# Performance work log

Hardware: AMD Instinct MI355X
Metric: run time of the kernel (lower is better)

The kernel has to match this reference:

```python
import jax, jax.numpy as jnp
import numpy as np

D_MODEL, N_HEADS, D_STATE, N_GROUPS, CHUNK = 2048, 32, 64, 1, 256
BATCH, SEQLEN = 2, 4096


def setup_inputs() -> dict:
    key = jax.random.key(0)
    ks = jax.random.split(key, 8)
    s = 0.02
    d, h, n, g = D_MODEL, N_HEADS, D_STATE, N_GROUPS
    return {
        "x": jax.random.normal(ks[0], (BATCH, SEQLEN, d), jnp.float32),
        "A_log": jnp.log(jnp.arange(1, h + 1, dtype=jnp.float32)),
        "D": jnp.ones((h,), jnp.float32),
        "B_w": jax.random.normal(ks[1], (g * n, d), jnp.float32) * s,
        "B_b": jnp.zeros((g * n,), jnp.float32),
        "C_w": jax.random.normal(ks[2], (g * n, d), jnp.float32) * s,
        "C_b": jnp.zeros((g * n,), jnp.float32),
        "dt_w": jax.random.normal(ks[3], (h, d), jnp.float32) * s,
        "dt_b": jnp.zeros((h,), jnp.float32),
        "out_w": jax.random.normal(ks[4], (d, d), jnp.float32) * s,
        "out_b": jnp.zeros((d,), jnp.float32),
    }


def segsum(v):
    # v: [..., T] -> [..., T, T]; out[i,j] = sum_{k=j+1..i} v[k] for i>=j, -inf else
    cs = jnp.cumsum(v, axis=-1)
    seg = cs[..., :, None] - cs[..., None, :]
    T = v.shape[-1]
    mask = jnp.tril(jnp.ones((T, T), bool))
    return jnp.where(mask, seg, -jnp.inf)


def _ssd(x, A_log, D, B_w, B_b, C_w, C_b, dt_w, dt_b, out_w, out_b):
    b, t, d = x.shape
    h = A_log.shape[0]
    n = B_w.shape[0] // N_GROUPS
    p = d // h
    l = CHUNK
    c = t // l

    A = -jnp.exp(A_log.astype(jnp.float32))                      # [h]
    B = (x @ B_w.T + B_b).reshape(b, t, N_GROUPS, n)             # g=1
    C = (x @ C_w.T + C_b).reshape(b, t, N_GROUPS, n)
    B = jnp.broadcast_to(B, (b, t, h, n))                        # repeat groups -> heads
    C = jnp.broadcast_to(C, (b, t, h, n))
    dt = jax.nn.softplus(x @ dt_w.T + dt_b)                      # [b,t,h]
    xh = x.reshape(b, t, h, p)

    # chunked SSD (Mamba2 mamba_chunk_scan_combined math)
    xc = xh.reshape(b, c, l, h, p)
    Bc = B.reshape(b, c, l, h, n)
    Cc = C.reshape(b, c, l, h, n)
    dtc = dt.reshape(b, c, l, h)
    dA = jnp.transpose(dtc * A, (0, 3, 1, 2))                    # [b,h,c,l]
    A_cumsum = jnp.cumsum(dA, axis=-1)                           # [b,h,c,l]

    # 1. intra-chunk (diagonal blocks)
    L = jnp.exp(segsum(dA))                                      # [b,h,c,l,l]
    xdt = xc * dtc[..., None]                                    # [b,c,l,h,p]
    Y_diag = jnp.einsum('bclhn,bcshn,bhcls,bcshp->bclhp', Cc, Bc, L, xdt)

    # 2. per-chunk final states
    decay_states = jnp.exp(A_cumsum[..., -1:] - A_cumsum)        # [b,h,c,l]
    states = jnp.einsum('bclhn,bhcl,bclhp->bchpn', Bc, decay_states, xdt)

    # 3. inter-chunk recurrence on chunk states
    states = jnp.concatenate([jnp.zeros_like(states[:, :1]), states], axis=1)  # [b,c+1,h,p,n]
    dA_last = jnp.pad(A_cumsum[..., -1], ((0, 0), (0, 0), (1, 0)))             # [b,h,c+1]
    decay_chunk = jnp.exp(segsum(dA_last))                                     # [b,h,c+1,c+1]
    new_states = jnp.einsum('bhzc,bchpn->bzhpn', decay_chunk, states)
    prev_states = new_states[:, :-1]                                           # [b,c,h,p,n]

    # 4. state -> output contribution
    state_decay_out = jnp.exp(A_cumsum)                          # [b,h,c,l]
    Y_off = jnp.einsum('bclhn,bchpn,bhcl->bclhp', Cc, prev_states, state_decay_out)

    Y = (Y_diag + Y_off).reshape(b, t, h, p) + D[None, None, :, None] * xh
    return Y.reshape(b, t, d) @ out_w.T + out_b


def reference(x, A_log, D, B_w, B_b, C_w, C_b, dt_w, dt_b, out_w, out_b):
    return _ssd(x, A_log, D, B_w, B_b, C_w, C_b, dt_w, dt_b, out_w, out_b)
```

## Files before the change

kernel.cpp:

```cpp
#include <hip/hip_runtime.h>
#include <hip/hip_bf16.h>
#include <math.h>

namespace {
constexpr int kDModel = 2048;
constexpr int kHeads  = 32;
constexpr int kState  = 64;
constexpr int kP      = 64;
constexpr int kChunk  = 256;
constexpr int kNChunk = 16;
constexpr int kBatch  = 2;
constexpr int kSeq    = 4096;
constexpr int kM      = kBatch * kSeq;
}

typedef __bf16 bf16_t;
typedef __attribute__((ext_vector_type(8))) __bf16 bf16x8;
typedef __attribute__((ext_vector_type(4))) __bf16 bf16x4;
typedef __attribute__((ext_vector_type(4))) float f32x4;

__device__ __forceinline__ void gload_lds16(const void* g, void* l) {
    __builtin_amdgcn_global_load_lds(
        (const __attribute__((address_space(1))) void*)g,
        (__attribute__((address_space(3))) void*)l,
        16, 0, 0);
}

__global__ __launch_bounds__(256)
void gemm_bcdt(const float* __restrict__ x, const bf16_t* __restrict__ W,
               const float* __restrict__ b0, const float* __restrict__ b1,
               const float* __restrict__ b2,
               bf16_t* __restrict__ o0h, bf16_t* __restrict__ o1h,
               float* __restrict__ o2f)
{
    constexpr int K = kDModel;
    constexpr int NT = K / 32;
    __shared__ float  Ast[3][256 * 4];
    __shared__ __bf16 Wst[3][768 * 8];
    const int tid  = threadIdx.x;
    const int lane = tid & 63;
    const int wave = tid >> 6;
    const int wm = (wave >> 1) * 16;
    const int wn = (wave & 1) * 80;
    const int l15 = lane & 15, quad = lane >> 4;
    const int m0 = blockIdx.x * 32;
    const int aks = tid >> 5, arow = tid & 31;

    auto stage = [&](int t2, int sb) {
        const int k0 = t2 * 32;
        gload_lds16(x + (size_t)(m0 + arow) * K + k0 + aks * 4, &Ast[sb][tid * 4]);
        #pragma unroll
        for (int e = 0; e < 3; ++e) {
            const int u = e * 256 + tid;
            const int ks = u / 192;
            const int n  = u - ks * 192;
            gload_lds16(W + (size_t)n * K + k0 + ks * 8, &Wst[sb][u * 8]);
        }
    };

    f32x4 acc[5];
    #pragma unroll
    for (int j = 0; j < 5; ++j) acc[j] = (f32x4){0.f, 0.f, 0.f, 0.f};

    stage(0, 0);
    stage(1, 1);
    asm volatile("s_waitcnt vmcnt(4)" ::: "memory");
    __builtin_amdgcn_s_barrier();

    int cur = 0;
    for (int t = 0; t < NT; ++t) {
        const float*  Ac = &Ast[cur][0];
        const __bf16* Wc = &Wst[cur][0];
        int stb = cur + 2; if (stb >= 3) stb -= 3;

        const float4 a0 = *reinterpret_cast<const float4*>(
            &Ac[((quad * 2 + 0) * 32 + wm + l15) * 4]);
        const float4 a1 = *reinterpret_cast<const float4*>(
            &Ac[((quad * 2 + 1) * 32 + wm + l15) * 4]);
        bf16x8 af;
        af[0] = (__bf16)a0.x; af[1] = (__bf16)a0.y;
        af[2] = (__bf16)a0.z; af[3] = (__bf16)a0.w;
        af[4] = (__bf16)a1.x; af[5] = (__bf16)a1.y;
        af[6] = (__bf16)a1.z; af[7] = (__bf16)a1.w;
        bf16x8 bfr[5];
        #pragma unroll
        for (int nf = 0; nf < 5; ++nf)
            bfr[nf] = *reinterpret_cast<const bf16x8*>(
                &Wc[(quad * 192 + wn + nf * 16 + l15) * 8]);
        if (t < NT - 2) stage(t + 2, stb);
        __builtin_amdgcn_s_setprio(1);
        #pragma unroll
        for (int nf = 0; nf < 5; ++nf)
            acc[nf] = __builtin_amdgcn_mfma_f32_16x16x32_bf16(af, bfr[nf], acc[nf], 0, 0, 0);
        __builtin_amdgcn_s_setprio(0);

        if (t < NT - 2) {
            asm volatile("s_waitcnt vmcnt(4)" ::: "memory");
        } else if (t < NT - 1) {
            asm volatile("s_waitcnt vmcnt(0)" ::: "memory");
        }
        if (t < NT - 1) __builtin_amdgcn_s_barrier();
        cur = cur + 1; if (cur == 3) cur = 0;
    }

    #pragma unroll
    for (int reg = 0; reg < 4; ++reg) {
        const int r = m0 + wm + quad * 4 + reg;
        #pragma unroll
        for (int nf = 0; nf < 5; ++nf) {
            const float v = acc[nf][reg];
            const int n = wn + nf * 16 + l15;
            if (n < 64) {
                o0h[(size_t)r * 64 + n] = (bf16_t)(v + b0[n]);
            } else if (n < 128) {
                o1h[(size_t)r * 64 + (n - 64)] = (bf16_t)(v + b1[n - 64]);
            } else {
                float z = v + b2[n - 128];
                o2f[(size_t)r * 32 + (n - 128)] = (z > 20.f) ? z : log1pf(expf(z));
            }
        }
    }
}

__global__ __launch_bounds__(512, 2)
void gemm256_out(const bf16_t* __restrict__ Ap, const bf16_t* __restrict__ Bp,
                 const float* __restrict__ bias, float* __restrict__ C)
{
    constexpr int M = 8192, N = 2048, NT = 2048 / 32;
    __shared__ __bf16 Ab[3][4 * 256 * 8];
    __shared__ __bf16 Bb[3][4 * 256 * 8];
    const int tid  = threadIdx.x;
    const int lane = tid & 63;
    const int wave = tid >> 6;
    const int l15 = lane & 15, quad = lane >> 4;
    const int bid = blockIdx.x;
    const int mt = (bid & 7) * 4 + ((bid >> 3) & 3);
    const int nt = bid >> 5;
    const int m0 = mt * 256;
    const int n0 = nt * 256;
    const int wm = (wave >> 2) * 128;
    const int wn = (wave & 3) * 64;

    const int u0 = tid, u1 = tid + 512;
    auto stage = [&](int t2, int stb) {
        const int ks0 = t2 * 4;
        const bf16_t* As = Ap + ((size_t)ks0 * M + m0) * 8;
        const bf16_t* Bs = Bp + ((size_t)ks0 * N + n0) * 8;
        __bf16* Al = &Ab[stb][0];
        __bf16* Bl = &Bb[stb][0];
        gload_lds16(As + ((size_t)(u0 >> 8) * M + (u0 & 255)) * 8, Al + u0 * 8);
        gload_lds16(As + ((size_t)(u1 >> 8) * M + (u1 & 255)) * 8, Al + u1 * 8);
        gload_lds16(Bs + ((size_t)(u0 >> 8) * N + (u0 & 255)) * 8, Bl + u0 * 8);
        gload_lds16(Bs + ((size_t)(u1 >> 8) * N + (u1 & 255)) * 8, Bl + u1 * 8);
    };

    f32x4 acc[8][4];
    #pragma unroll
    for (int i = 0; i < 8; ++i)
        #pragma unroll
        for (int j = 0; j < 4; ++j)
            acc[i][j] = (f32x4){0.f, 0.f, 0.f, 0.f};

    stage(0, 0);
    stage(1, 1);
    asm volatile("s_waitcnt vmcnt(4)" ::: "memory");
    __builtin_amdgcn_s_barrier();

    int cur = 0;
    for (int t = 0; t < NT; ++t) {
        const __bf16* Ac = &Ab[cur][0];
        const __bf16* Bc = &Bb[cur][0];
        int stb = cur + 2; if (stb >= 3) stb -= 3;

        bf16x8 af[4], bfr[4];
        #pragma unroll
        for (int mi = 0; mi < 4; ++mi)
            af[mi] = *reinterpret_cast<const bf16x8*>(
                &Ac[(quad * 256 + wm + mi * 16 + l15) * 8]);
        #pragma unroll
        for (int nj = 0; nj < 4; ++nj)
            bfr[nj] = *reinterpret_cast<const bf16x8*>(
                &Bc[(quad * 256 + wn + nj * 16 + l15) * 8]);
        if (t < NT - 2) stage(t + 2, stb);
        __builtin_amdgcn_s_setprio(1);
        #pragma unroll
        for (int mi = 0; mi < 4; ++mi)
            #pragma unroll
            for (int nj = 0; nj < 4; ++nj)
                acc[mi][nj] = __builtin_amdgcn_mfma_f32_16x16x32_bf16(
                    af[mi], bfr[nj], acc[mi][nj], 0, 0, 0);
        __builtin_amdgcn_s_setprio(0);

        #pragma unroll
        for (int mi = 0; mi < 4; ++mi)
            af[mi] = *reinterpret_cast<const bf16x8*>(
                &Ac[(quad * 256 + wm + 64 + mi * 16 + l15) * 8]);
        __builtin_amdgcn_s_setprio(1);
        #pragma unroll
        for (int mi = 0; mi < 4; ++mi)
            #pragma unroll
            for (int nj = 0; nj < 4; ++nj)
                acc[4 + mi][nj] = __builtin_amdgcn_mfma_f32_16x16x32_bf16(
                    af[mi], bfr[nj], acc[4 + mi][nj], 0, 0, 0);
        __builtin_amdgcn_s_setprio(0);

        if (t < NT - 2) {
            asm volatile("s_waitcnt vmcnt(4)" ::: "memory");
        } else if (t < NT - 1) {
            asm volatile("s_waitcnt vmcnt(0)" ::: "memory");
        }
        if (t < NT - 1) __builtin_amdgcn_s_barrier();
        cur = cur + 1; if (cur == 3) cur = 0;
    }

    float bia[4];
    #pragma unroll
    for (int nj = 0; nj < 4; ++nj) bia[nj] = bias[n0 + wn + nj * 16 + l15];
    #pragma unroll
    for (int mi = 0; mi < 8; ++mi) {
        #pragma unroll
        for (int reg = 0; reg < 4; ++reg) {
            const int r = m0 + wm + mi * 16 + quad * 4 + reg;
            #pragma unroll
            for (int nj = 0; nj < 4; ++nj) {
                const int c = n0 + wn + nj * 16 + l15;
                C[(size_t)r * N + c] = acc[mi][nj][reg] + bia[nj];
            }
        }
    }
}

__global__ __launch_bounds__(256)
void prep_fused(const float* __restrict__ W, bf16_t* __restrict__ Wp,
                const float* __restrict__ B_w, const float* __restrict__ C_w,
                const float* __restrict__ dt_w, bf16_t* __restrict__ wcat)
{
    const int bid = blockIdx.x;
    if (bid < 2048) {
        const int idx = bid * 256 + threadIdx.x;
        const int n = idx >> 8, ks = idx & 255;
        const float4 v0 = *reinterpret_cast<const float4*>(W + (size_t)n * 2048 + ks * 8);
        const float4 v1 = *reinterpret_cast<const float4*>(W + (size_t)n * 2048 + ks * 8 + 4);
        bf16x8 o;
        o[0] = (__bf16)v0.x; o[1] = (__bf16)v0.y; o[2] = (__bf16)v0.z; o[3] = (__bf16)v0.w;
        o[4] = (__bf16)v1.x; o[5] = (__bf16)v1.y; o[6] = (__bf16)v1.z; o[7] = (__bf16)v1.w;
        *reinterpret_cast<bf16x8*>(Wp + ((size_t)ks * 2048 + n) * 8) = o;
    } else {
        const int idx = (bid - 2048) * 256 + threadIdx.x;
        const int r = idx >> 11, k = idx & 2047;
        float v = 0.f;
        if (r < 64)       v = B_w[r * 2048 + k];
        else if (r < 128) v = C_w[(r - 64) * 2048 + k];
        else if (r < 160) v = dt_w[(r - 128) * 2048 + k];
        wcat[idx] = (bf16_t)v;
    }
}

__global__ __launch_bounds__(256)
void mid_fused(const float* __restrict__ dtm, const float* __restrict__ A_log,
               float* __restrict__ Acs, const bf16_t* __restrict__ Bb16,
               bf16_t* __restrict__ bTg, const float* __restrict__ x,
               bf16_t* __restrict__ xdtT)
{
    const int bid = blockIdx.x;
    const int tid = threadIdx.x;
    if (bid < 1024) {
        const int ci = bid & (kNChunk - 1);
        const int hi = (bid >> 4) & (kHeads - 1);
        const int bi = bid >> 9;
        const float Ah = -expf(A_log[hi]);
        __shared__ float s[kChunk];
        s[tid] = dtm[((size_t)bi * kSeq + ci * kChunk + tid) * kHeads + hi] * Ah;
        __syncthreads();
        for (int off = 1; off < kChunk; off <<= 1) {
            const float add = (tid >= off) ? s[tid - off] : 0.f;
            __syncthreads();
            s[tid] += add;
            __syncthreads();
        }
        Acs[((size_t)(bi * kHeads + hi) * kNChunk + ci) * kChunk + tid] = s[tid];
    } else if (bid < 1024 + 32) {
        const int blk = bid - 1024;
        const int ci = blk & (kNChunk - 1);
        const int bi = blk >> 4;
        const size_t rowbase = (size_t)bi * kSeq + ci * kChunk;
        __shared__ __bf16 T[64 * 264];
        bf16x8 v[8];
        #pragma unroll
        for (int e = 0; e < 8; ++e)
            v[e] = *reinterpret_cast<const bf16x8*>(Bb16 + (rowbase + tid) * 64 + e * 8);
        #pragma unroll
        for (int e = 0; e < 8; ++e)
            #pragma unroll
            for (int j = 0; j < 8; ++j)
                T[(e * 8 + j) * 264 + tid] = v[e][j];
        __syncthreads();
        const int n = tid >> 2, seg = (tid & 3) * 64;
        bf16_t* dst = bTg + ((size_t)(bi * kNChunk + ci)) * (64 * 256) + n * 256 + seg;
        #pragma unroll
        for (int j = 0; j < 8; ++j) {
            *reinterpret_cast<bf16x8*>(dst + j * 8) =
                *reinterpret_cast<const bf16x8*>(&T[n * 264 + seg + j * 8]);
        }
    } else {
        const int blk = bid - 1024 - 32;
        const int hi = blk & (kHeads - 1);
        const int ci = (blk >> 5) & (kNChunk - 1);
        const int bi = blk >> 9;
        const size_t rowbase = (size_t)bi * kSeq + ci * kChunk;
        __shared__ __bf16 T[64 * 264];
        const float d = dtm[(rowbase + tid) * kHeads + hi];
        const float* xs = x + (rowbase + tid) * kDModel + hi * kP;
        #pragma unroll
        for (int e = 0; e < 8; ++e) {
            const float4 a = *reinterpret_cast<const float4*>(xs + e * 8);
            const float4 b = *reinterpret_cast<const float4*>(xs + e * 8 + 4);
            T[(e * 8 + 0) * 264 + tid] = (__bf16)(a.x * d);
            T[(e * 8 + 1) * 264 + tid] = (__bf16)(a.y * d);
            T[(e * 8 + 2) * 264 + tid] = (__bf16)(a.z * d);
            T[(e * 8 + 3) * 264 + tid] = (__bf16)(a.w * d);
            T[(e * 8 + 4) * 264 + tid] = (__bf16)(b.x * d);
            T[(e * 8 + 5) * 264 + tid] = (__bf16)(b.y * d);
            T[(e * 8 + 6) * 264 + tid] = (__bf16)(b.z * d);
            T[(e * 8 + 7) * 264 + tid] = (__bf16)(b.w * d);
        }
        __syncthreads();
        const int p = tid >> 2, seg = (tid & 3) * 64;
        bf16_t* dst = xdtT + (size_t)blk * (64 * 256) + p * 256 + seg;
        #pragma unroll
        for (int j = 0; j < 8; ++j) {
            *reinterpret_cast<bf16x8*>(dst + j * 8) =
                *reinterpret_cast<const bf16x8*>(&T[p * 264 + seg + j * 8]);
        }
    }
}

__global__ __launch_bounds__(256)
void states_mfma(const bf16_t* __restrict__ xdtT, const bf16_t* __restrict__ bTg,
                 const float* __restrict__ Acs, float* __restrict__ states)
{
    const int blk = blockIdx.x;
    const int hi = blk & (kHeads - 1);
    const int ci = (blk >> 5) & (kNChunk - 1);
    const int bi = blk >> 9;
    __shared__ __bf16 Xa[64 * 264];
    __shared__ __bf16 Bt[64 * 264];
    __shared__ float dec[kChunk];
    const int tid = threadIdx.x;
    const int lane = tid & 63;
    const int wave = tid >> 6;
    const int l15 = lane & 15, quad = lane >> 4;

    const float* acs = Acs + ((size_t)(bi * kHeads + hi) * kNChunk + ci) * kChunk;
    dec[tid] = expf(acs[kChunk - 1] - acs[tid]);
    __syncthreads();

    const bf16_t* bsrc = bTg + ((size_t)(bi * kNChunk + ci)) * (64 * 256);
    const bf16_t* xsrc = xdtT + (size_t)blk * (64 * 256);
    #pragma unroll
    for (int e = 0; e < 8; ++e) {
        const int u = e * 256 + tid;
        const int r = u >> 5, seg = (u & 31) * 8;
        *reinterpret_cast<bf16x8*>(&Bt[r * 264 + seg]) =
            *reinterpret_cast<const bf16x8*>(bsrc + r * 256 + seg);
        bf16x8 xv = *reinterpret_cast<const bf16x8*>(xsrc + r * 256 + seg);
        bf16x8 xo;
        #pragma unroll
        for (int j = 0; j < 8; ++j)
            xo[j] = (__bf16)((float)xv[j] * dec[seg + j]);
        *reinterpret_cast<bf16x8*>(&Xa[r * 264 + seg]) = xo;
    }
    __syncthreads();

    f32x4 acc[4];
    #pragma unroll
    for (int ni = 0; ni < 4; ++ni) acc[ni] = (f32x4){0.f, 0.f, 0.f, 0.f};
    #pragma unroll
    for (int kk = 0; kk < 8; ++kk) {
        const bf16x8 af = *reinterpret_cast<const bf16x8*>(
            &Xa[(wave * 16 + l15) * 264 + kk * 32 + quad * 8]);
        #pragma unroll
        for (int ni = 0; ni < 4; ++ni) {
            const bf16x8 bf = *reinterpret_cast<const bf16x8*>(
                &Bt[(ni * 16 + l15) * 264 + kk * 32 + quad * 8]);
            acc[ni] = __builtin_amdgcn_mfma_f32_16x16x32_bf16(af, bf, acc[ni], 0, 0, 0);
        }
    }
    float* sp = states + (size_t)blk * (kP * kState);
    #pragma unroll
    for (int reg = 0; reg < 4; ++reg) {
        const int p = wave * 16 + quad * 4 + reg;
        #pragma unroll
        for (int ni = 0; ni < 4; ++ni)
            sp[(size_t)p * kState + ni * 16 + l15] = acc[ni][reg];
    }
}

__global__ __launch_bounds__(256)
void chunkscan_kernel(const float* __restrict__ states, const float* __restrict__ Acs,
                      bf16_t* __restrict__ prevsb)
{
    const int q  = blockIdx.x & 15;
    const int hi = (blockIdx.x >> 4) & (kHeads - 1);
    const int bi = blockIdx.x >> 9;
    const int e  = q * 256 + threadIdx.x;
    __shared__ float ea[kNChunk];
    if (threadIdx.x < kNChunk)
        ea[threadIdx.x] = expf(Acs[((size_t)(bi * kHeads + hi) * kNChunk + threadIdx.x)
                                   * kChunk + kChunk - 1]);
    __syncthreads();
    float P = 0.f;
    prevsb[((size_t)(bi * kNChunk + 0) * kHeads + hi) * (kP * kState) + e] = (bf16_t)0.f;
    for (int c = 1; c < kNChunk; ++c) {
        P = fmaf(ea[c - 1], P,
                 states[((size_t)(bi * kNChunk + (c - 1)) * kHeads + hi) * (kP * kState) + e]);
        prevsb[((size_t)(bi * kNChunk + c) * kHeads + hi) * (kP * kState) + e] = (bf16_t)P;
    }
}

__global__ __launch_bounds__(256)
void ychunk_mfma(const bf16_t* __restrict__ Bb16, const bf16_t* __restrict__ Cb16,
                 const bf16_t* __restrict__ xdtT, const float* __restrict__ Acs,
                 const bf16_t* __restrict__ prevsb, const float* __restrict__ dtm,
                 const float* __restrict__ Dvec, bf16_t* __restrict__ Yp)
{
    const int blk = blockIdx.x;
    const int lt = blk & 3;
    const int hi = (blk >> 2) & (kHeads - 1);
    const int ci = (blk >> 7) & (kNChunk - 1);
    const int bi = blk >> 11;
    __shared__ float acs_s[kChunk];
    __shared__ float dts_s[64];
    __shared__ __bf16 Cs[64 * 72];
    __shared__ __bf16 Bs[64 * 72];
    __shared__ __bf16 Xt[64 * 72];
    __shared__ __bf16 Sp[64 * 72];
    const int tid = threadIdx.x;
    const int lane = tid & 63;
    const int wave = tid >> 6;
    const int l15 = lane & 15, quad = lane >> 4;
    const int mrow = wave * 16 + quad * 4;
    const size_t rowbase = (size_t)bi * kSeq + ci * kChunk;
    const bf16_t* xdsrc = xdtT + ((size_t)((bi * kNChunk + ci) * kHeads + hi)) * (64 * 256);
    const int ur0 = tid >> 3,          useg0 = (tid & 7) * 8;
    const int ur1 = (256 + tid) >> 3,  useg1 = (tid & 7) * 8;

    acs_s[tid] = Acs[((size_t)(bi * kHeads + hi) * kNChunk + ci) * kChunk + tid];
    if (tid < 64) dts_s[tid] = dtm[(rowbase + lt * 64 + tid) * kHeads + hi];
    const bf16_t* pp = prevsb + ((size_t)(bi * kNChunk + ci) * kHeads + hi) * (kP * kState);
    #pragma unroll
    for (int e = 0; e < 2; ++e) {
        const int r = e ? ur1 : ur0, seg = e ? useg1 : useg0;
        *reinterpret_cast<bf16x8*>(&Cs[r * 72 + seg]) =
            *reinterpret_cast<const bf16x8*>(Cb16 + (rowbase + lt * 64 + r) * 64 + seg);
        *reinterpret_cast<bf16x8*>(&Bs[r * 72 + seg]) =
            *reinterpret_cast<const bf16x8*>(pp + r * 64 + seg);
    }
    bf16x8 rB0, rB1, rX0, rX1;
    rB0 = *reinterpret_cast<const bf16x8*>(Bb16 + (rowbase + ur0) * 64 + useg0);
    rB1 = *reinterpret_cast<const bf16x8*>(Bb16 + (rowbase + ur1) * 64 + useg1);
    rX0 = *reinterpret_cast<const bf16x8*>(xdsrc + ur0 * 256 + useg0);
    rX1 = *reinterpret_cast<const bf16x8*>(xdsrc + ur1 * 256 + useg1);
    __syncthreads();

    bf16x8 af[2];
    af[0] = *reinterpret_cast<const bf16x8*>(&Cs[(wave * 16 + l15) * 72 + quad * 8]);
    af[1] = *reinterpret_cast<const bf16x8*>(&Cs[(wave * 16 + l15) * 72 + 32 + quad * 8]);

    f32x4 yacc[4];
    #pragma unroll
    for (int ni = 0; ni < 4; ++ni) yacc[ni] = (f32x4){0.f, 0.f, 0.f, 0.f};
    #pragma unroll
    for (int ni = 0; ni < 4; ++ni) {
        const bf16x8 b0 = *reinterpret_cast<const bf16x8*>(&Bs[(ni * 16 + l15) * 72 + quad * 8]);
        const bf16x8 b1 = *reinterpret_cast<const bf16x8*>(&Bs[(ni * 16 + l15) * 72 + 32 + quad * 8]);
        yacc[ni] = __builtin_amdgcn_mfma_f32_16x16x32_bf16(af[0], b0, yacc[ni], 0, 0, 0);
        yacc[ni] = __builtin_amdgcn_mfma_f32_16x16x32_bf16(af[1], b1, yacc[ni], 0, 0, 0);
    }
    {
        float es[4];
        #pragma unroll
        for (int reg = 0; reg < 4; ++reg) es[reg] = expf(acs_s[lt * 64 + mrow + reg]);
        #pragma unroll
        for (int ni = 0; ni < 4; ++ni)
            #pragma unroll
            for (int reg = 0; reg < 4; ++reg) yacc[ni][reg] *= es[reg];
    }

    for (int st = 0; st <= lt; ++st) {
        __syncthreads();
        *reinterpret_cast<bf16x8*>(&Bs[ur0 * 72 + useg0]) = rB0;
        *reinterpret_cast<bf16x8*>(&Bs[ur1 * 72 + useg1]) = rB1;
        *reinterpret_cast<bf16x8*>(&Xt[ur0 * 72 + useg0]) = rX0;
        *reinterpret_cast<bf16x8*>(&Xt[ur1 * 72 + useg1]) = rX1;
        if (st < lt) {
            rB0 = *reinterpret_cast<const bf16x8*>(Bb16 + (rowbase + (st + 1) * 64 + ur0) * 64 + useg0);
            rB1 = *reinterpret_cast<const bf16x8*>(Bb16 + (rowbase + (st + 1) * 64 + ur1) * 64 + useg1);
            rX0 = *reinterpret_cast<const bf16x8*>(xdsrc + ur0 * 256 + (st + 1) * 64 + useg0);
            rX1 = *reinterpret_cast<const bf16x8*>(xdsrc + ur1 * 256 + (st + 1) * 64 + useg1);
        }
        __syncthreads();
        f32x4 sacc[4];
        #pragma unroll
        for (int ni = 0; ni < 4; ++ni) sacc[ni] = (f32x4){0.f, 0.f, 0.f, 0.f};
        #pragma unroll
        for (int ni = 0; ni < 4; ++ni) {
            const bf16x8 b0 = *reinterpret_cast<const bf16x8*>(&Bs[(ni * 16 + l15) * 72 + quad * 8]);
            const bf16x8 b1 = *reinterpret_cast<const bf16x8*>(&Bs[(ni * 16 + l15) * 72 + 32 + quad * 8]);
            sacc[ni] = __builtin_amdgcn_mfma_f32_16x16x32_bf16(af[0], b0, sacc[ni], 0, 0, 0);
            sacc[ni] = __builtin_amdgcn_mfma_f32_16x16x32_bf16(af[1], b1, sacc[ni], 0, 0, 0);
        }
        #pragma unroll
        for (int reg = 0; reg < 4; ++reg) {
            const int l = lt * 64 + mrow + reg;
            const float al = acs_s[l];
            #pragma unroll
            for (int ni = 0; ni < 4; ++ni) {
                const int scol = ni * 16 + l15;
                const int sg = st * 64 + scol;
                float v = sacc[ni][reg] * expf(al - acs_s[sg]);
                if (st == lt && sg > l) v = 0.f;
                Sp[(mrow + reg) * 72 + scol] = (__bf16)v;
            }
        }
        asm volatile("s_waitcnt lgkmcnt(0)" ::: "memory");
        __builtin_amdgcn_sched_barrier(0);
        const bf16x8 as0 = *reinterpret_cast<const bf16x8*>(&Sp[(wave * 16 + l15) * 72 + quad * 8]);
        const bf16x8 as1 = *reinterpret_cast<const bf16x8*>(&Sp[(wave * 16 + l15) * 72 + 32 + quad * 8]);
        #pragma unroll
        for (int ni = 0; ni < 4; ++ni) {
            const bf16x8 x0 = *reinterpret_cast<const bf16x8*>(&Xt[(ni * 16 + l15) * 72 + quad * 8]);
            const bf16x8 x1 = *reinterpret_cast<const bf16x8*>(&Xt[(ni * 16 + l15) * 72 + 32 + quad * 8]);
            yacc[ni] = __builtin_amdgcn_mfma_f32_16x16x32_bf16(as0, x0, yacc[ni], 0, 0, 0);
            yacc[ni] = __builtin_amdgcn_mfma_f32_16x16x32_bf16(as1, x1, yacc[ni], 0, 0, 0);
        }
    }

    const float Dh = Dvec[hi];
    #pragma unroll
    for (int reg = 0; reg < 4; ++reg) {
        const int lrow = mrow + reg;
        const size_t tg = rowbase + lt * 64 + lrow;
        const float dinv = 1.f / dts_s[lrow];
        #pragma unroll
        for (int ni = 0; ni < 4; ++ni) {
            const int p = ni * 16 + l15;
            const float xv = (float)Xt[p * 72 + lrow] * dinv;
            const float v = yacc[ni][reg] + Dh * xv;
            Yp[((size_t)(hi * 8 + (p >> 3)) * (size_t)kM + tg) * 8 + (p & 7)] = (bf16_t)v;
        }
    }
}

extern "C" void kernel_launch(void* const* d_in, const int* in_sizes, int n_in,
                              void* d_out, int out_size, void* d_ws, size_t ws_size,
                              hipStream_t stream)
{
    (void)in_sizes; (void)n_in; (void)out_size; (void)ws_size;
    const float* x     = (const float*)d_in[0];
    const float* A_log = (const float*)d_in[1];
    const float* Dvec  = (const float*)d_in[2];
    const float* B_w   = (const float*)d_in[3];
    const float* B_b   = (const float*)d_in[4];
    const float* C_w   = (const float*)d_in[5];
    const float* C_b   = (const float*)d_in[6];
    const float* dt_w  = (const float*)d_in[7];
    const float* dt_b  = (const float*)d_in[8];
    const float* out_w = (const float*)d_in[9];
    const float* out_b = (const float*)d_in[10];
    float* out = (float*)d_out;

    float* ws = (float*)d_ws;
    float* dtm    = ws;
    float* Acs    = dtm + (size_t)kM * kHeads;
    float* states = Acs + (size_t)kBatch * kHeads * kNChunk * kChunk;
    bf16_t* prevsb = (bf16_t*)(states + (size_t)kBatch * kNChunk * kHeads * kP * kState);
    bf16_t* Y     = prevsb + (size_t)kBatch * kNChunk * kHeads * kP * kState;
    bf16_t* Bb16  = Y + (size_t)kM * kDModel;
    bf16_t* Cb16  = Bb16 + (size_t)kM * kState;
    bf16_t* xdtT  = Cb16 + (size_t)kM * kState;
    bf16_t* bTg   = xdtT + (size_t)kM * kDModel;
    bf16_t* wcat  = bTg + (size_t)kBatch * kNChunk * kState * kChunk;
    bf16_t* wob   = wcat + (size_t)192 * kDModel;

    const dim3 blk(256);
    prep_fused<<<dim3(2048 + 1536), blk, 0, stream>>>(out_w, wob, B_w, C_w, dt_w, wcat);
    gemm_bcdt<<<dim3(kM / 32), blk, 0, stream>>>(x, wcat, B_b, C_b, dt_b,
                                                 Bb16, Cb16, dtm);
    mid_fused<<<dim3(1024 + 32 + 1024), blk, 0, stream>>>(
        dtm, A_log, Acs, Bb16, bTg, x, xdtT);
    states_mfma<<<dim3(kBatch * kNChunk * kHeads), blk, 0, stream>>>(xdtT, bTg, Acs, states);
    chunkscan_kernel<<<dim3(kBatch * kHeads * 16), blk, 0, stream>>>(states, Acs, prevsb);
    ychunk_mfma<<<dim3(kBatch * kNChunk * kHeads * 4), blk, 0, stream>>>(
        Bb16, Cb16, xdtT, Acs, prevsb, dtm, Dvec, Y);
    gemm256_out<<<dim3(256), dim3(512), 0, stream>>>(Y, wob, out_b, out);
}
```

Before: 350.6 us.

## Merge four ychunk row-tile blocks into one 512-thread block sharing B/X tiles

ychunk_mfma now launches one 512-thread block per (batch, chunk, head) instead of four 256-thread blocks, one per 64-row tile. Each pair of waves owns one 64-row tile. The B and xdt tiles for each source sub-chunk are staged into LDS once and shared by all row tiles, which removes the redundant global loads the separate blocks used to make. The C tile buffer is reused as the scratch for the masked score matrix. In exchange, waves for early row tiles sit idle through later source steps but still hit every barrier, and the grid has four times fewer blocks.

```diff
diff --git a/kernel.cpp b/kernel.cpp
--- a/kernel.cpp
+++ b/kernel.cpp
@@ -418,136 +418,158 @@
     }
 }
 
-__global__ __launch_bounds__(256)
+__global__ __launch_bounds__(512)
 void ychunk_mfma(const bf16_t* __restrict__ Bb16, const bf16_t* __restrict__ Cb16,
                  const bf16_t* __restrict__ xdtT, const float* __restrict__ Acs,
                  const bf16_t* __restrict__ prevsb, const float* __restrict__ dtm,
                  const float* __restrict__ Dvec, bf16_t* __restrict__ Yp)
 {
     const int blk = blockIdx.x;
-    const int lt = blk & 3;
-    const int hi = (blk >> 2) & (kHeads - 1);
-    const int ci = (blk >> 7) & (kNChunk - 1);
-    const int bi = blk >> 11;
+    const int hi = blk & (kHeads - 1);
+    const int ci = (blk >> 5) & (kNChunk - 1);
+    const int bi = blk >> 9;
     __shared__ float acs_s[kChunk];
-    __shared__ float dts_s[64];
-    __shared__ __bf16 Cs[64 * 72];
-    __shared__ __bf16 Bs[64 * 72];
+    __shared__ float dts_s[kChunk];
+    __shared__ __bf16 CsSp[256 * 72];
+    __shared__ __bf16 BsPs[64 * 72];
     __shared__ __bf16 Xt[64 * 72];
-    __shared__ __bf16 Sp[64 * 72];
     const int tid = threadIdx.x;
     const int lane = tid & 63;
     const int wave = tid >> 6;
+    const int lt   = wave >> 1;
+    const int half = wave & 1;
     const int l15 = lane & 15, quad = lane >> 4;
-    const int mrow = wave * 16 + quad * 4;
+    const int rbase = lt * 64 + half * 32;
     const size_t rowbase = (size_t)bi * kSeq + ci * kChunk;
-    const bf16_t* xdsrc = xdtT + ((size_t)((bi * kNChunk + ci) * kHeads + hi)) * (64 * 256);
-    const int ur0 = tid >> 3,          useg0 = (tid & 7) * 8;
-    const int ur1 = (256 + tid) >> 3,  useg1 = (tid & 7) * 8;
-
-    acs_s[tid] = Acs[((size_t)(bi * kHeads + hi) * kNChunk + ci) * kChunk + tid];
-    if (tid < 64) dts_s[tid] = dtm[(rowbase + lt * 64 + tid) * kHeads + hi];
+    const bf16_t* xdsrc = xdtT + (size_t)blk * (64 * 256);
+    const int ur = tid >> 3, useg = (tid & 7) * 8;
+
+    if (tid < 256) acs_s[tid] = Acs[((size_t)(bi * kHeads + hi) * kNChunk + ci) * kChunk + tid];
+    else           dts_s[tid - 256] = dtm[(rowbase + tid - 256) * kHeads + hi];
+    #pragma unroll
+    for (int e = 0; e < 4; ++e) {
+        const int u = e * 512 + tid;
+        const int r = u >> 3, seg = (u & 7) * 8;
+        *reinterpret_cast<bf16x8*>(&CsSp[r * 72 + seg]) =
+            *reinterpret_cast<const bf16x8*>(Cb16 + (rowbase + r) * 64 + seg);
+    }
     const bf16_t* pp = prevsb + ((size_t)(bi * kNChunk + ci) * kHeads + hi) * (kP * kState);
-    #pragma unroll
-    for (int e = 0; e < 2; ++e) {
-        const int r = e ? ur1 : ur0, seg = e ? useg1 : useg0;
-        *reinterpret_cast<bf16x8*>(&Cs[r * 72 + seg]) =
-            *reinterpret_cast<const bf16x8*>(Cb16 + (rowbase + lt * 64 + r) * 64 + seg);
-        *reinterpret_cast<bf16x8*>(&Bs[r * 72 + seg]) =
-            *reinterpret_cast<const bf16x8*>(pp + r * 64 + seg);
-    }
-    bf16x8 rB0, rB1, rX0, rX1;
-    rB0 = *reinterpret_cast<const bf16x8*>(Bb16 + (rowbase + ur0) * 64 + useg0);
-    rB1 = *reinterpret_cast<const bf16x8*>(Bb16 + (rowbase + ur1) * 64 + useg1);
-    rX0 = *reinterpret_cast<const bf16x8*>(xdsrc + ur0 * 256 + useg0);
-    rX1 = *reinterpret_cast<const bf16x8*>(xdsrc + ur1 * 256 + useg1);
+    *reinterpret_cast<bf16x8*>(&BsPs[ur * 72 + useg]) =
+        *reinterpret_cast<const bf16x8*>(pp + ur * 64 + useg);
+    bf16x8 rB, rX;
+    rB = *reinterpret_cast<const bf16x8*>(Bb16 + (rowbase + ur) * 64 + useg);
+    rX = *reinterpret_cast<const bf16x8*>(xdsrc + ur * 256 + useg);
     __syncthreads();
 
-    bf16x8 af[2];
-    af[0] = *reinterpret_cast<const bf16x8*>(&Cs[(wave * 16 + l15) * 72 + quad * 8]);
-    af[1] = *reinterpret_cast<const bf16x8*>(&Cs[(wave * 16 + l15) * 72 + 32 + quad * 8]);
-
-    f32x4 yacc[4];
-    #pragma unroll
-    for (int ni = 0; ni < 4; ++ni) yacc[ni] = (f32x4){0.f, 0.f, 0.f, 0.f};
+    bf16x8 af[2][2];
+    #pragma unroll
+    for (int mi = 0; mi < 2; ++mi) {
+        af[mi][0] = *reinterpret_cast<const bf16x8*>(&CsSp[(rbase + mi * 16 + l15) * 72 + quad * 8]);
+        af[mi][1] = *reinterpret_cast<const bf16x8*>(&CsSp[(rbase + mi * 16 + l15) * 72 + 32 + quad * 8]);
+    }
+
+    f32x4 yacc[2][4];
+    #pragma unroll
+    for (int mi = 0; mi < 2; ++mi)
+        #pragma unroll
+        for (int ni = 0; ni < 4; ++ni) yacc[mi][ni] = (f32x4){0.f, 0.f, 0.f, 0.f};
     #pragma unroll
     for (int ni = 0; ni < 4; ++ni) {
-        const bf16x8 b0 = *reinterpret_cast<const bf16x8*>(&Bs[(ni * 16 + l15) * 72 + quad * 8]);
-        const bf16x8 b1 = *reinterpret_cast<const bf16x8*>(&Bs[(ni * 16 + l15) * 72 + 32 + quad * 8]);
-        yacc[ni] = __builtin_amdgcn_mfma_f32_16x16x32_bf16(af[0], b0, yacc[ni], 0, 0, 0);
-        yacc[ni] = __builtin_amdgcn_mfma_f32_16x16x32_bf16(af[1], b1, yacc[ni], 0, 0, 0);
-    }
-    {
+        const bf16x8 b0 = *reinterpret_cast<const bf16x8*>(&BsPs[(ni * 16 + l15) * 72 + quad * 8]);
+        const bf16x8 b1 = *reinterpret_cast<const bf16x8*>(&BsPs[(ni * 16 + l15) * 72 + 32 + quad * 8]);
+        #pragma unroll
+        for (int mi = 0; mi < 2; ++mi) {
+            yacc[mi][ni] = __builtin_amdgcn_mfma_f32_16x16x32_bf16(af[mi][0], b0, yacc[mi][ni], 0, 0, 0);
+            yacc[mi][ni] = __builtin_amdgcn_mfma_f32_16x16x32_bf16(af[mi][1], b1, yacc[mi][ni], 0, 0, 0);
+        }
+    }
+    #pragma unroll
+    for (int mi = 0; mi < 2; ++mi) {
         float es[4];
         #pragma unroll
-        for (int reg = 0; reg < 4; ++reg) es[reg] = expf(acs_s[lt * 64 + mrow + reg]);
+        for (int reg = 0; reg < 4; ++reg)
+            es[reg] = expf(acs_s[rbase + mi * 16 + quad * 4 + reg]);
         #pragma unroll
         for (int ni = 0; ni < 4; ++ni)
             #pragma unroll
-            for (int reg = 0; reg < 4; ++reg) yacc[ni][reg] *= es[reg];
-    }
-
-    for (int st = 0; st <= lt; ++st) {
+            for (int reg = 0; reg < 4; ++reg) yacc[mi][ni][reg] *= es[reg];
+    }
+
+    const float Dh = Dvec[hi];
+    for (int st = 0; st < 4; ++st) {
         __syncthreads();
-        *reinterpret_cast<bf16x8*>(&Bs[ur0 * 72 + useg0]) = rB0;
-        *reinterpret_cast<bf16x8*>(&Bs[ur1 * 72 + useg1]) = rB1;
-        *reinterpret_cast<bf16x8*>(&Xt[ur0 * 72 + useg0]) = rX0;
-        *reinterpret_cast<bf16x8*>(&Xt[ur1 * 72 + useg1]) = rX1;
-        if (st < lt) {
-            rB0 = *reinterpret_cast<const bf16x8*>(Bb16 + (rowbase + (st + 1) * 64 + ur0) * 64 + useg0);
-            rB1 = *reinterpret_cast<const bf16x8*>(Bb16 + (rowbase + (st + 1) * 64 + ur1) * 64 + useg1);
-            rX0 = *reinterpret_cast<const bf16x8*>(xdsrc + ur0 * 256 + (st + 1) * 64 + useg0);
-            rX1 = *reinterpret_cast<const bf16x8*>(xdsrc + ur1 * 256 + (st + 1) * 64 + useg1);
+        *reinterpret_cast<bf16x8*>(&BsPs[ur * 72 + useg]) = rB;
+        *reinterpret_cast<bf16x8*>(&Xt[ur * 72 + useg])   = rX;
+        if (st < 3) {
+            rB = *reinterpret_cast<const bf16x8*>(Bb16 + (rowbase + (st + 1) * 64 + ur) * 64 + useg);
+            rX = *reinterpret_cast<const bf16x8*>(xdsrc + ur * 256 + (st + 1) * 64 + useg);
         }
         __syncthreads();
-        f32x4 sacc[4];
-        #pragma unroll
-        for (int ni = 0; ni < 4; ++ni) sacc[ni] = (f32x4){0.f, 0.f, 0.f, 0.f};
-        #pragma unroll
-        for (int ni = 0; ni < 4; ++ni) {
-            const bf16x8 b0 = *reinterpret_cast<const bf16x8*>(&Bs[(ni * 16 + l15) * 72 + quad * 8]);
-            const bf16x8 b1 = *reinterpret_cast<const bf16x8*>(&Bs[(ni * 16 + l15) * 72 + 32 + quad * 8]);
-            sacc[ni] = __builtin_amdgcn_mfma_f32_16x16x32_bf16(af[0], b0, sacc[ni], 0, 0, 0);
-            sacc[ni] = __builtin_amdgcn_mfma_f32_16x16x32_bf16(af[1], b1, sacc[ni], 0, 0, 0);
-        }
-        #pragma unroll
-        for (int reg = 0; reg < 4; ++reg) {
-            const int l = lt * 64 + mrow + reg;
-            const float al = acs_s[l];
+        if (lt >= st) {
+            f32x4 sacc[2][4];
+            #pragma unroll
+            for (int mi = 0; mi < 2; ++mi)
+                #pragma unroll
+                for (int ni = 0; ni < 4; ++ni) sacc[mi][ni] = (f32x4){0.f, 0.f, 0.f, 0.f};
             #pragma unroll
             for (int ni = 0; ni < 4; ++ni) {
-                const int scol = ni * 16 + l15;
-                const int sg = st * 64 + scol;
-                float v = sacc[ni][reg] * expf(al - acs_s[sg]);
-                if (st == lt && sg > l) v = 0.f;
-                Sp[(mrow + reg) * 72 + scol] = (__bf16)v;
+                const bf16x8 b0 = *reinterpret_cast<const bf16x8*>(&BsPs[(ni * 16 + l15) * 72 + quad * 8]);
+                const bf16x8 b1 = *reinterpret_cast<const bf16x8*>(&BsPs[(ni * 16 + l15) * 72 + 32 + quad * 8]);
+                #pragma unroll
+                for (int mi = 0; mi < 2; ++mi) {
+                    sacc[mi][ni] = __builtin_amdgcn_mfma_f32_16x16x32_bf16(af[mi][0], b0, sacc[mi][ni], 0, 0, 0);
+                    sacc[mi][ni] = __builtin_amdgcn_mfma_f32_16x16x32_bf16(af[mi][1], b1, sacc[mi][ni], 0, 0, 0);
+                }
             }
-        }
-        asm volatile("s_waitcnt lgkmcnt(0)" ::: "memory");
-        __builtin_amdgcn_sched_barrier(0);
-        const bf16x8 as0 = *reinterpret_cast<const bf16x8*>(&Sp[(wave * 16 + l15) * 72 + quad * 8]);
-        const bf16x8 as1 = *reinterpret_cast<const bf16x8*>(&Sp[(wave * 16 + l15) * 72 + 32 + quad * 8]);
-        #pragma unroll
-        for (int ni = 0; ni < 4; ++ni) {
-            const bf16x8 x0 = *reinterpret_cast<const bf16x8*>(&Xt[(ni * 16 + l15) * 72 + quad * 8]);
-            const bf16x8 x1 = *reinterpret_cast<const bf16x8*>(&Xt[(ni * 16 + l15) * 72 + 32 + quad * 8]);
-            yacc[ni] = __builtin_amdgcn_mfma_f32_16x16x32_bf16(as0, x0, yacc[ni], 0, 0, 0);
-            yacc[ni] = __builtin_amdgcn_mfma_f32_16x16x32_bf16(as1, x1, yacc[ni], 0, 0, 0);
-        }
-    }
-
-    const float Dh = Dvec[hi];
-    #pragma unroll
-    for (int reg = 0; reg < 4; ++reg) {
-        const int lrow = mrow + reg;
-        const size_t tg = rowbase + lt * 64 + lrow;
-        const float dinv = 1.f / dts_s[lrow];
-        #pragma unroll
-        for (int ni = 0; ni < 4; ++ni) {
-            const int p = ni * 16 + l15;
-            const float xv = (float)Xt[p * 72 + lrow] * dinv;
-            const float v = yacc[ni][reg] + Dh * xv;
-            Yp[((size_t)(hi * 8 + (p >> 3)) * (size_t)kM + tg) * 8 + (p & 7)] = (bf16_t)v;
+            #pragma unroll
+            for (int mi = 0; mi < 2; ++mi) {
+                #pragma unroll
+                for (int reg = 0; reg < 4; ++reg) {
+                    const int rloc = rbase + mi * 16 + quad * 4 + reg;
+                    const int l = lt * 64 + (rloc - lt * 64);
+                    const float al = acs_s[rloc];
+                    #pragma unroll
+                    for (int ni = 0; ni < 4; ++ni) {
+                        const int scol = ni * 16 + l15;
+                        const int sg = st * 64 + scol;
+                        float v = sacc[mi][ni][reg] * expf(al - acs_s[sg]);
+                        if (st == lt && sg > l) v = 0.f;
+                        CsSp[rloc * 72 + scol] = (__bf16)v;
+                    }
+                }
+            }
+            asm volatile("s_waitcnt lgkmcnt(0)" ::: "memory");
+            __builtin_amdgcn_sched_barrier(0);
+            #pragma unroll
+            for (int mi = 0; mi < 2; ++mi) {
+                const bf16x8 as0 = *reinterpret_cast<const bf16x8*>(&CsSp[(rbase + mi * 16 + l15) * 72 + quad * 8]);
+                const bf16x8 as1 = *reinterpret_cast<const bf16x8*>(&CsSp[(rbase + mi * 16 + l15) * 72 + 32 + quad * 8]);
+                #pragma unroll
+                for (int ni = 0; ni < 4; ++ni) {
+                    const bf16x8 x0 = *reinterpret_cast<const bf16x8*>(&Xt[(ni * 16 + l15) * 72 + quad * 8]);
+                    const bf16x8 x1 = *reinterpret_cast<const bf16x8*>(&Xt[(ni * 16 + l15) * 72 + 32 + quad * 8]);
+                    yacc[mi][ni] = __builtin_amdgcn_mfma_f32_16x16x32_bf16(as0, x0, yacc[mi][ni], 0, 0, 0);
+                    yacc[mi][ni] = __builtin_amdgcn_mfma_f32_16x16x32_bf16(as1, x1, yacc[mi][ni], 0, 0, 0);
+                }
+            }
+            if (lt == st) {
+                #pragma unroll
+                for (int mi = 0; mi < 2; ++mi) {
+                    #pragma unroll
+                    for (int reg = 0; reg < 4; ++reg) {
+                        const int lrow = half * 32 + mi * 16 + quad * 4 + reg;
+                        const size_t tg = rowbase + lt * 64 + lrow;
+                        const float dinv = 1.f / dts_s[lt * 64 + lrow];
+                        #pragma unroll
+                        for (int ni = 0; ni < 4; ++ni) {
+                            const int p = ni * 16 + l15;
+                            const float xv = (float)Xt[p * 72 + lrow] * dinv;
+                            const float v = yacc[mi][ni][reg] + Dh * xv;
+                            Yp[((size_t)(hi * 8 + (p >> 3)) * (size_t)kM + tg) * 8 + (p & 7)] = (bf16_t)v;
+                        }
+                    }
+                }
+            }
         }
     }
 }
@@ -591,7 +613,7 @@
         dtm, A_log, Acs, Bb16, bTg, x, xdtT);
     states_mfma<<<dim3(kBatch * kNChunk * kHeads), blk, 0, stream>>>(xdtT, bTg, Acs, states);
     chunkscan_kernel<<<dim3(kBatch * kHeads * 16), blk, 0, stream>>>(states, Acs, prevsb);
-    ychunk_mfma<<<dim3(kBatch * kNChunk * kHeads * 4), blk, 0, stream>>>(
+    ychunk_mfma<<<dim3(kBatch * kNChunk * kHeads), dim3(512), 0, stream>>>(
         Bb16, Cb16, xdtT, Acs, prevsb, dtm, Dvec, Y);
     gemm256_out<<<dim3(256), dim3(512), 0, stream>>>(Y, wob, out_b, out);
 }
```

Result: no change. 355.5 us (+1.4%).
